# Optimization experiments

Measured on AMD Instinct MI355X. Metric: run time of the kernel, lower is better.

The kernel has to match this reference:

```python
import jax, jax.numpy as jnp
import numpy as np

N, DIM1, DIM2 = 4096, 512, 128

def setup_inputs() -> dict:
    key = jax.random.key(0)
    kx, kw = jax.random.split(key)
    X = jax.random.normal(kx, (N, DIM1), dtype=jnp.float32)
    # original module initializes weight to ones; use randn-scaled for a
    # non-degenerate correctness baseline is NOT faithful -> keep ones.
    weight = jnp.ones((DIM2, DIM1, DIM1), dtype=jnp.float32)
    return {"X": X, "weight": weight}

def reference(X, weight):
    # Y[n,k] = x_n^T W_k x_n  == diagonal of X @ W_k @ X^T, computed directly
    # without materializing the NxN matrix.
    XW = jnp.einsum('ni,kij->nkj', X, weight)   # [N, dim2, dim1]
    Y = jnp.einsum('nkj,nj->nk', XW, X)         # [N, dim2]
    return Y
```

## Files before the change

### kernel.cpp

```cpp
#include <hip/hip_runtime.h>

#define D1 512
#define K2 128

typedef __bf16 bf16_t;
typedef bf16_t bf16x8 __attribute__((ext_vector_type(8)));
typedef bf16_t bf16x4 __attribute__((ext_vector_type(4)));
typedef float  f32x4  __attribute__((ext_vector_type(4)));
typedef float  f32x16 __attribute__((ext_vector_type(16)));

#define WBF_OFF 0ull
#define XBF_OFF 67108864ull
#define WS_NEED 71303168ull

__global__ __launch_bounds__(256)
void prep_w(const float* __restrict__ W, bf16_t* __restrict__ Wbf)
{
    const int k  = blockIdx.x >> 4;
    const int is = blockIdx.x & 15;
    const int t  = threadIdx.x;
    __shared__ float lt[16384];
    char* ltb = (char*)lt;
    {
        const int r  = t >> 3;
        const int cb = (t & 7) * 64;
        const float* src = W + ((size_t)k * D1 + is * 32 + r) * D1 + cb;
        const int sw = (r & 15) << 4;
        #pragma unroll
        for (int c = 0; c < 16; ++c) {
            float4 v = *reinterpret_cast<const float4*>(src + c * 4);
            *reinterpret_cast<float4*>(ltb + r * 2048 + (((cb + c * 4) * 4) ^ sw)) = v;
        }
    }
    __syncthreads();
    bf16_t* out = Wbf + ((size_t)k * 16 + is) * 16384;
    #pragma unroll
    for (int p = 0; p < 8; ++p) {
        const int cc = p * 256 + t;
        const int s  = cc >> 6;
        const int l2 = cc & 63;
        const int il = l2 & 31;
        const int jb = s * 16 + (l2 >> 5) * 8;
        const int sw = (il & 15) << 4;
        bf16x8 h;
        #pragma unroll
        for (int e = 0; e < 8; ++e) {
            float v = *reinterpret_cast<const float*>(ltb + il * 2048 + (((jb + e) * 4) ^ sw));
            h[e] = (bf16_t)v;
        }
        *reinterpret_cast<bf16x8*>(out + (size_t)cc * 8) = h;
    }
}

__global__ __launch_bounds__(256)
void prep_x(const float* __restrict__ X, bf16_t* __restrict__ Xbf)
{
    const int nb2 = blockIdx.x >> 2;
    const int jc  = blockIdx.x & 3;
    const int t   = threadIdx.x;
    __shared__ float xt[16384];
    {
        const int nl = t >> 1;
        const int cb = (t & 1) * 64;
        const float* src = X + ((size_t)nb2 * 128 + nl) * D1 + jc * 128 + cb;
        #pragma unroll
        for (int c = 0; c < 16; ++c) {
            float4 v = *reinterpret_cast<const float4*>(src + c * 4);
            *reinterpret_cast<float4*>(&xt[nl * 128 + cb + c * 4]) = v;
        }
    }
    __syncthreads();
    bf16_t* outx = Xbf + ((size_t)nb2 * 4 + jc) * 16384;
    #pragma unroll
    for (int p = 0; p < 8; ++p) {
        const int cc   = p * 256 + t;
        const int n    = cc >> 4;
        const int slot = cc & 15;
        const int j8   = slot ^ (n & 15);
        bf16x8 h;
        #pragma unroll
        for (int e = 0; e < 8; ++e) h[e] = (bf16_t)xt[n * 128 + j8 * 8 + e];
        *reinterpret_cast<bf16x8*>(outx + (size_t)cc * 8) = h;
    }
}

__global__ __launch_bounds__(512, 2)
void tr_main(const bf16_t* __restrict__ Wbf, const bf16_t* __restrict__ Xbf,
             float* __restrict__ Y)
{
    extern __shared__ char smem[];
    float* red = (float*)(smem + 131072);

    const int bid = blockIdx.x;
    const int k   = ((bid >> 8) << 3) + (bid & 7);
    const int nb2 = (bid >> 3) & 31;

    const int tid = threadIdx.x;
    const int w   = tid >> 6;
    const int l   = tid & 63;
    const int l31 = l & 31;
    const int lh  = l >> 5;

    {
        const bf16_t* src = Xbf + (size_t)nb2 * 65536;
        bf16x8 tmp[16];
        #pragma unroll
        for (int jc = 0; jc < 4; ++jc)
            #pragma unroll
            for (int p = 0; p < 4; ++p) {
                const int ci = (p * 8 + w) * 64 + l;
                tmp[jc * 4 + p] = *reinterpret_cast<const bf16x8*>(
                    src + (size_t)jc * 16384 + (size_t)ci * 8);
            }
        #pragma unroll
        for (int jc = 0; jc < 4; ++jc)
            #pragma unroll
            for (int p = 0; p < 4; ++p) {
                const int ci = (p * 8 + w) * 64 + l;
                *reinterpret_cast<bf16x8*>(smem + jc * 32768 + ci * 16) = tmp[jc * 4 + p];
            }
    }
    __syncthreads();

    const bf16_t* A0 = Wbf + ((size_t)k * 16 + w * 2) * 16384 + (size_t)l * 8;
    const int sw = (l & 15) << 4;

    f32x16 acc[2][4] = {};

    bf16x8 Aq[2][2];
    #pragma unroll
    for (int d = 0; d < 2; ++d) {
        Aq[d][0] = *reinterpret_cast<const bf16x8*>(A0 + (size_t)d * 512);
        Aq[d][1] = *reinterpret_cast<const bf16x8*>(A0 + 16384 + (size_t)d * 512);
    }

    auto bread = [&](bf16x8* dst, int s) {
        const int slot = s >> 3;
        const int ct   = ((s & 7) * 32 + lh * 16) ^ sw;
        #pragma unroll
        for (int fn = 0; fn < 4; ++fn)
            dst[fn] = *reinterpret_cast<const bf16x8*>(
                smem + slot * 32768 + (fn * 32 + l31) * 256 + ct);
    };

    bf16x8 B[2][4];
    bread(B[0], 0);

    #pragma unroll
    for (int s = 0; s < 32; ++s) {
        const int qi = s & 1;
        bf16x8 a0 = Aq[qi][0];
        bf16x8 a1 = Aq[qi][1];
        if (s + 2 < 32) {
            Aq[qi][0] = *reinterpret_cast<const bf16x8*>(A0 + (size_t)(s + 2) * 512);
            Aq[qi][1] = *reinterpret_cast<const bf16x8*>(A0 + 16384 + (size_t)(s + 2) * 512);
        }
        if (s < 31) bread(B[(s + 1) & 1], s + 1);
        __builtin_amdgcn_s_setprio(1);
        #pragma unroll
        for (int fn = 0; fn < 4; ++fn) {
            acc[0][fn] = __builtin_amdgcn_mfma_f32_32x32x16_bf16(a0, B[qi][fn], acc[0][fn], 0, 0, 0);
            acc[1][fn] = __builtin_amdgcn_mfma_f32_32x32x16_bf16(a1, B[qi][fn], acc[1][fn], 0, 0, 0);
        }
        __builtin_amdgcn_s_setprio(0);
    }

    float yp[4] = {0.f, 0.f, 0.f, 0.f};
    #pragma unroll
    for (int mi = 0; mi < 2; ++mi) {
        const int strip = w * 2 + mi;
        const char* base = smem + ((strip >> 2) & 3) * 32768;
        #pragma unroll
        for (int rq = 0; rq < 4; ++rq) {
            const int slot = (strip * 4 + rq) & 15;
            #pragma unroll
            for (int fn = 0; fn < 4; ++fn) {
                const int n = fn * 32 + l31;
                bf16x4 xv = *reinterpret_cast<const bf16x4*>(
                    base + n * 256 + ((slot ^ (n & 15)) << 4) + lh * 8);
                #pragma unroll
                for (int q = 0; q < 4; ++q)
                    yp[fn] += acc[mi][fn][rq * 4 + q] * (float)xv[q];
            }
        }
    }
    #pragma unroll
    for (int fn = 0; fn < 4; ++fn) {
        float v = yp[fn];
        v += __shfl_down(v, 32);
        if (lh == 0) red[w * 128 + fn * 32 + l31] = v;
    }
    __syncthreads();
    if (tid < 128) {
        float s2 = 0.f;
        #pragma unroll
        for (int w2 = 0; w2 < 8; ++w2) s2 += red[w2 * 128 + tid];
        Y[((size_t)nb2 * 128 + tid) * K2 + k] = s2;
    }
}

__global__ __launch_bounds__(512, 2)
void tensor_reduction_kernel(const float* __restrict__ X,
                             const float* __restrict__ W,
                             float* __restrict__ Y)
{
    const int bid = blockIdx.x;
    const int xcd = bid & 7;
    const int rr_ = bid >> 3;
    const int kk  = xcd + 8 * (rr_ >> 4);
    const int nb  = (rr_ & 15) * 256;

    const int tid = threadIdx.x;
    const int wv  = tid >> 6;
    const int ln  = tid & 63;
    const int lg  = ln >> 4;
    const int lr  = ln & 15;

    __shared__ __align__(16) bf16_t Xs[256 * 64];
    __shared__ __align__(16) bf16_t Ws[2][64 * 64];

    bf16x8 afrag[2][16];
    {
        const int srow = tid >> 4;
        const int sj4  = (tid & 15) * 4;
        #pragma unroll
        for (int c = 0; c < 8; ++c) {
            #pragma unroll
            for (int p = 0; p < 8; ++p) {
                const int row = p * 32 + srow;
                float4 v = *reinterpret_cast<const float4*>(
                    X + (size_t)(nb + row) * D1 + c * 64 + sj4);
                bf16x4 h = { (bf16_t)v.x, (bf16_t)v.y, (bf16_t)v.z, (bf16_t)v.w };
                const int byte = row * 128 + ((sj4 * 2) ^ ((row & 7) << 4));
                *reinterpret_cast<bf16x4*>((char*)Xs + byte) = h;
            }
            __syncthreads();
            #pragma unroll
            for (int m = 0; m < 2; ++m) {
                #pragma unroll
                for (int ks = 0; ks < 2; ++ks) {
                    const int row  = wv * 32 + m * 16 + lr;
                    const int byte = row * 128 + ((ks * 64 + lg * 16) ^ ((row & 7) << 4));
                    afrag[m][2 * c + ks] =
                        *reinterpret_cast<const bf16x8*>((const char*)Xs + byte);
                }
            }
            __syncthreads();
        }
    }

    const float* Wk  = W + (size_t)kk * D1 * D1;
    const int irow = tid >> 3;
    const int j8   = (tid & 7) * 8;

    float ypart[2][4] = {{0.f,0.f,0.f,0.f},{0.f,0.f,0.f,0.f}};

    {
        const float* src = Wk + (size_t)irow * D1 + j8;
        float4 u0 = *reinterpret_cast<const float4*>(src);
        float4 u1 = *reinterpret_cast<const float4*>(src + 4);
        bf16x8 h = { (bf16_t)u0.x,(bf16_t)u0.y,(bf16_t)u0.z,(bf16_t)u0.w,
                     (bf16_t)u1.x,(bf16_t)u1.y,(bf16_t)u1.z,(bf16_t)u1.w };
        const int byte = irow * 128 + ((j8 * 2) ^ ((irow & 7) << 4));
        *reinterpret_cast<bf16x8*>((char*)Ws[0] + byte) = h;
    }
    __syncthreads();

    for (int it = 0; it < 8; ++it) {
        f32x4 acc[2][4] = {};
        #pragma unroll
        for (int jcc = 0; jcc < 8; ++jcc) {
            const int tI  = it * 8 + jcc;
            const int cur = tI & 1;
            float4 u0, u1;
            const bool pf = (tI < 63);
            if (pf) {
                const int nit = (tI + 1) >> 3, njc = (tI + 1) & 7;
                const float* src = Wk + (size_t)(nit * 64 + irow) * D1 + njc * 64 + j8;
                u0 = *reinterpret_cast<const float4*>(src);
                u1 = *reinterpret_cast<const float4*>(src + 4);
            }
            #pragma unroll
            for (int ks = 0; ks < 2; ++ks) {
                bf16x8 bfr[4];
                #pragma unroll
                for (int f = 0; f < 4; ++f) {
                    const int ir   = f * 16 + lr;
                    const int byte = ir * 128 + ((ks * 64 + lg * 16) ^ ((ir & 7) << 4));
                    bfr[f] = *reinterpret_cast<const bf16x8*>((const char*)Ws[cur] + byte);
                }
                #pragma unroll
                for (int m = 0; m < 2; ++m)
                    #pragma unroll
                    for (int f = 0; f < 4; ++f)
                        acc[m][f] = __builtin_amdgcn_mfma_f32_16x16x32_bf16(
                            afrag[m][2 * jcc + ks], bfr[f], acc[m][f], 0, 0, 0);
            }
            if (pf) {
                bf16x8 h = { (bf16_t)u0.x,(bf16_t)u0.y,(bf16_t)u0.z,(bf16_t)u0.w,
                             (bf16_t)u1.x,(bf16_t)u1.y,(bf16_t)u1.z,(bf16_t)u1.w };
                const int byte = irow * 128 + ((j8 * 2) ^ ((irow & 7) << 4));
                *reinterpret_cast<bf16x8*>((char*)Ws[cur ^ 1] + byte) = h;
            }
            __syncthreads();
        }
        #pragma unroll
        for (int m = 0; m < 2; ++m) {
            #pragma unroll
            for (int f = 0; f < 4; ++f) {
                const int col = it * 64 + f * 16 + lr;
                #pragma unroll
                for (int q = 0; q < 4; ++q) {
                    const int grow = nb + wv * 32 + m * 16 + lg * 4 + q;
                    ypart[m][q] += acc[m][f][q] * X[(size_t)grow * D1 + col];
                }
            }
        }
    }

    #pragma unroll
    for (int m = 0; m < 2; ++m) {
        #pragma unroll
        for (int q = 0; q < 4; ++q) {
            float v = ypart[m][q];
            v += __shfl_xor(v, 1, 64);
            v += __shfl_xor(v, 2, 64);
            v += __shfl_xor(v, 4, 64);
            v += __shfl_xor(v, 8, 64);
            if (lr == 0) {
                const int grow = nb + wv * 32 + m * 16 + lg * 4 + q;
                Y[(size_t)grow * K2 + kk] = v;
            }
        }
    }
}

extern "C" void kernel_launch(void* const* d_in, const int* in_sizes, int n_in,
                              void* d_out, int out_size, void* d_ws, size_t ws_size,
                              hipStream_t stream)
{
    const float* X = (const float*)d_in[0];
    const float* W = (const float*)d_in[1];
    float* Y = (float*)d_out;

    if (d_ws != nullptr && ws_size >= WS_NEED) {
        bf16_t* Wbf = (bf16_t*)((char*)d_ws + WBF_OFF);
        bf16_t* Xbf = (bf16_t*)((char*)d_ws + XBF_OFF);
        prep_w<<<2048, 256, 0, stream>>>(W, Wbf);
        prep_x<<<128, 256, 0, stream>>>(X, Xbf);
        (void)hipFuncSetAttribute((const void*)tr_main,
                                  hipFuncAttributeMaxDynamicSharedMemorySize, 135168);
        tr_main<<<4096, 512, 135168, stream>>>(Wbf, Xbf, Y);
    } else {
        tensor_reduction_kernel<<<2048, 512, 0, stream>>>(X, W, Y);
    }
}
```

Baseline: 282.6 us.

## Halve tr_main N tile to 64 rows to raise occupancy

Shrinks each tr_main block from 128 to 64 X rows, halving LDS usage and accumulators, doubling the grid to 8192 blocks and raising launch bounds to 4 blocks per CU. The aim is to fit more blocks per CU and hide load latency better. In exchange each bf16 weight tile is reused across half as many rows, so total weight traffic from cache/HBM doubles.

```diff
diff --git a/kernel.cpp b/kernel.cpp
--- a/kernel.cpp
+++ b/kernel.cpp
@@ -84,16 +84,16 @@
     }
 }
 
-__global__ __launch_bounds__(512, 2)
+__global__ __launch_bounds__(512, 4)
 void tr_main(const bf16_t* __restrict__ Wbf, const bf16_t* __restrict__ Xbf,
              float* __restrict__ Y)
 {
     extern __shared__ char smem[];
-    float* red = (float*)(smem + 131072);
+    float* red = (float*)(smem + 65536);
 
     const int bid = blockIdx.x;
-    const int k   = ((bid >> 8) << 3) + (bid & 7);
-    const int nb2 = (bid >> 3) & 31;
+    const int k   = (bid & 7) + ((bid >> 9) << 3);
+    const int nb  = (bid >> 3) & 63;
 
     const int tid = threadIdx.x;
     const int w   = tid >> 6;
@@ -102,22 +102,22 @@
     const int lh  = l >> 5;
 
     {
-        const bf16_t* src = Xbf + (size_t)nb2 * 65536;
-        bf16x8 tmp[16];
+        const bf16_t* src = Xbf + (size_t)(nb >> 1) * 65536 + (size_t)(nb & 1) * 8192;
+        bf16x8 tmp[8];
         #pragma unroll
         for (int jc = 0; jc < 4; ++jc)
             #pragma unroll
-            for (int p = 0; p < 4; ++p) {
-                const int ci = (p * 8 + w) * 64 + l;
-                tmp[jc * 4 + p] = *reinterpret_cast<const bf16x8*>(
+            for (int p = 0; p < 2; ++p) {
+                const int ci = p * 512 + tid;
+                tmp[jc * 2 + p] = *reinterpret_cast<const bf16x8*>(
                     src + (size_t)jc * 16384 + (size_t)ci * 8);
             }
         #pragma unroll
         for (int jc = 0; jc < 4; ++jc)
             #pragma unroll
-            for (int p = 0; p < 4; ++p) {
-                const int ci = (p * 8 + w) * 64 + l;
-                *reinterpret_cast<bf16x8*>(smem + jc * 32768 + ci * 16) = tmp[jc * 4 + p];
+            for (int p = 0; p < 2; ++p) {
+                const int ci = p * 512 + tid;
+                *reinterpret_cast<bf16x8*>(smem + jc * 16384 + ci * 16) = tmp[jc * 2 + p];
             }
     }
     __syncthreads();
@@ -125,7 +125,7 @@
     const bf16_t* A0 = Wbf + ((size_t)k * 16 + w * 2) * 16384 + (size_t)l * 8;
     const int sw = (l & 15) << 4;
 
-    f32x16 acc[2][4] = {};
+    f32x16 acc[2][2] = {};
 
     bf16x8 Aq[2][2];
     #pragma unroll
@@ -134,16 +134,16 @@
         Aq[d][1] = *reinterpret_cast<const bf16x8*>(A0 + 16384 + (size_t)d * 512);
     }
 
-    auto bread = [&](bf16x8* dst, int s) {
-        const int slot = s >> 3;
-        const int ct   = ((s & 7) * 32 + lh * 16) ^ sw;
-        #pragma unroll
-        for (int fn = 0; fn < 4; ++fn)
+    auto bread = [&](bf16x8* dst, int su) {
+        const char* base = smem + (su >> 3) * 16384;
+        const int ct = ((((su & 7) * 2 + lh) << 4)) ^ sw;
+        #pragma unroll
+        for (int fn = 0; fn < 2; ++fn)
             dst[fn] = *reinterpret_cast<const bf16x8*>(
-                smem + slot * 32768 + (fn * 32 + l31) * 256 + ct);
+                base + (fn * 32 + l31) * 256 + ct);
     };
 
-    bf16x8 B[2][4];
+    bf16x8 B[2][2];
     bread(B[0], 0);
 
     #pragma unroll
@@ -157,24 +157,23 @@
         }
         if (s < 31) bread(B[(s + 1) & 1], s + 1);
         __builtin_amdgcn_s_setprio(1);
-        #pragma unroll
-        for (int fn = 0; fn < 4; ++fn) {
-            acc[0][fn] = __builtin_amdgcn_mfma_f32_32x32x16_bf16(a0, B[qi][fn], acc[0][fn], 0, 0, 0);
-            acc[1][fn] = __builtin_amdgcn_mfma_f32_32x32x16_bf16(a1, B[qi][fn], acc[1][fn], 0, 0, 0);
-        }
+        acc[0][0] = __builtin_amdgcn_mfma_f32_32x32x16_bf16(a0, B[qi][0], acc[0][0], 0, 0, 0);
+        acc[0][1] = __builtin_amdgcn_mfma_f32_32x32x16_bf16(a0, B[qi][1], acc[0][1], 0, 0, 0);
+        acc[1][0] = __builtin_amdgcn_mfma_f32_32x32x16_bf16(a1, B[qi][0], acc[1][0], 0, 0, 0);
+        acc[1][1] = __builtin_amdgcn_mfma_f32_32x32x16_bf16(a1, B[qi][1], acc[1][1], 0, 0, 0);
         __builtin_amdgcn_s_setprio(0);
     }
 
-    float yp[4] = {0.f, 0.f, 0.f, 0.f};
+    float yp[2] = {0.f, 0.f};
     #pragma unroll
     for (int mi = 0; mi < 2; ++mi) {
-        const int strip = w * 2 + mi;
-        const char* base = smem + ((strip >> 2) & 3) * 32768;
+        const int st32 = w * 2 + mi;
+        const char* base = smem + (st32 >> 2) * 16384;
         #pragma unroll
         for (int rq = 0; rq < 4; ++rq) {
-            const int slot = (strip * 4 + rq) & 15;
-            #pragma unroll
-            for (int fn = 0; fn < 4; ++fn) {
+            const int slot = (st32 * 4 + rq) & 15;
+            #pragma unroll
+            for (int fn = 0; fn < 2; ++fn) {
                 const int n = fn * 32 + l31;
                 bf16x4 xv = *reinterpret_cast<const bf16x4*>(
                     base + n * 256 + ((slot ^ (n & 15)) << 4) + lh * 8);
@@ -185,17 +184,17 @@
         }
     }
     #pragma unroll
-    for (int fn = 0; fn < 4; ++fn) {
+    for (int fn = 0; fn < 2; ++fn) {
         float v = yp[fn];
         v += __shfl_down(v, 32);
-        if (lh == 0) red[w * 128 + fn * 32 + l31] = v;
-    }
-    __syncthreads();
-    if (tid < 128) {
+        if (lh == 0) red[w * 64 + fn * 32 + l31] = v;
+    }
+    __syncthreads();
+    if (tid < 64) {
         float s2 = 0.f;
         #pragma unroll
-        for (int w2 = 0; w2 < 8; ++w2) s2 += red[w2 * 128 + tid];
-        Y[((size_t)nb2 * 128 + tid) * K2 + k] = s2;
+        for (int w2 = 0; w2 < 8; ++w2) s2 += red[w2 * 64 + tid];
+        Y[((size_t)nb * 64 + tid) * K2 + k] = s2;
     }
 }
 
@@ -349,8 +348,8 @@
         prep_w<<<2048, 256, 0, stream>>>(W, Wbf);
         prep_x<<<128, 256, 0, stream>>>(X, Xbf);
         (void)hipFuncSetAttribute((const void*)tr_main,
-                                  hipFuncAttributeMaxDynamicSharedMemorySize, 135168);
-        tr_main<<<4096, 512, 135168, stream>>>(Wbf, Xbf, Y);
+                                  hipFuncAttributeMaxDynamicSharedMemorySize, 67584);
+        tr_main<<<8192, 512, 67584, stream>>>(Wbf, Xbf, Y);
     } else {
         tensor_reduction_kernel<<<2048, 512, 0, stream>>>(X, W, Y);
     }
```

Result: no change. 278.8 us (-1.3%).

## Double-buffer X tiles via direct global-to-LDS loads, halving shared memory

Applied to the files above, without the earlier changes.

The main kernel stops staging the whole 128KB X tile in LDS up front. It streams 32KB X chunks into two LDS buffers using global_load_lds and overlaps those loads with MFMA work on the other buffer. Each wave now handles one 32-row strip at a time, two sequential passes with an accumulator reset and fold in between, so register use drops and launch bounds allow 4 blocks per CU instead of 2. This trades extra barriers, per-step W loads with no register prefetch, and repeated B reads from LDS for higher occupancy and less upfront load latency.

```diff
diff --git a/kernel.cpp b/kernel.cpp
--- a/kernel.cpp
+++ b/kernel.cpp
@@ -12,6 +12,10 @@
 #define WBF_OFF 0ull
 #define XBF_OFF 67108864ull
 #define WS_NEED 71303168ull
+
+#define GLOAD_LDS16(g, l)  __builtin_amdgcn_global_load_lds(              \
+    (__attribute__((address_space(1))) void*)(g),                         \
+    (__attribute__((address_space(3))) void*)(l), 16, 0, 0)
 
 __global__ __launch_bounds__(256)
 void prep_w(const float* __restrict__ W, bf16_t* __restrict__ Wbf)
@@ -84,106 +88,107 @@
     }
 }
 
-__global__ __launch_bounds__(512, 2)
+__global__ __launch_bounds__(512, 4)
 void tr_main(const bf16_t* __restrict__ Wbf, const bf16_t* __restrict__ Xbf,
              float* __restrict__ Y)
 {
     extern __shared__ char smem[];
-    float* red = (float*)(smem + 131072);
+    float* red = (float*)(smem + 65536);
 
     const int bid = blockIdx.x;
-    const int k   = ((bid >> 8) << 3) + (bid & 7);
-    const int nb2 = (bid >> 3) & 31;
+    const int k   = (bid & 7) + 8 * (bid >> 8);
+    const int nt  = (bid >> 3) & 31;
 
     const int tid = threadIdx.x;
     const int w   = tid >> 6;
     const int l   = tid & 63;
     const int l31 = l & 31;
     const int lh  = l >> 5;
-
-    {
-        const bf16_t* src = Xbf + (size_t)nb2 * 65536;
-        bf16x8 tmp[16];
-        #pragma unroll
-        for (int jc = 0; jc < 4; ++jc)
-            #pragma unroll
-            for (int p = 0; p < 4; ++p) {
-                const int ci = (p * 8 + w) * 64 + l;
-                tmp[jc * 4 + p] = *reinterpret_cast<const bf16x8*>(
-                    src + (size_t)jc * 16384 + (size_t)ci * 8);
-            }
-        #pragma unroll
-        for (int jc = 0; jc < 4; ++jc)
-            #pragma unroll
-            for (int p = 0; p < 4; ++p) {
-                const int ci = (p * 8 + w) * 64 + l;
-                *reinterpret_cast<bf16x8*>(smem + jc * 32768 + ci * 16) = tmp[jc * 4 + p];
-            }
-    }
-    __syncthreads();
-
-    const bf16_t* A0 = Wbf + ((size_t)k * 16 + w * 2) * 16384 + (size_t)l * 8;
-    const int sw = (l & 15) << 4;
-
-    f32x16 acc[2][4] = {};
-
-    bf16x8 Aq[2][2];
-    #pragma unroll
-    for (int d = 0; d < 2; ++d) {
-        Aq[d][0] = *reinterpret_cast<const bf16x8*>(A0 + (size_t)d * 512);
-        Aq[d][1] = *reinterpret_cast<const bf16x8*>(A0 + 16384 + (size_t)d * 512);
-    }
-
-    auto bread = [&](bf16x8* dst, int s) {
-        const int slot = s >> 3;
-        const int ct   = ((s & 7) * 32 + lh * 16) ^ sw;
-        #pragma unroll
-        for (int fn = 0; fn < 4; ++fn)
-            dst[fn] = *reinterpret_cast<const bf16x8*>(
-                smem + slot * 32768 + (fn * 32 + l31) * 256 + ct);
+    const int sw  = (l & 15) << 4;
+
+    const bf16_t* xsrc = Xbf + (size_t)nt * 65536;
+
+    f32x16 acc[4];
+    float  yp[4] = {0.f, 0.f, 0.f, 0.f};
+
+    auto stage = [&](int jc, int buf) {
+        const bf16_t* src = xsrc + (size_t)jc * 16384;
+        char* ldsb = smem + buf * 32768;
+        #pragma unroll
+        for (int q = 0; q < 4; ++q) {
+            const int cb = (q * 8 + w) * 64;
+            GLOAD_LDS16(src + (size_t)(cb + l) * 8, ldsb + (size_t)cb * 16);
+        }
     };
 
-    bf16x8 B[2][4];
-    bread(B[0], 0);
-
-    #pragma unroll
-    for (int s = 0; s < 32; ++s) {
-        const int qi = s & 1;
-        bf16x8 a0 = Aq[qi][0];
-        bf16x8 a1 = Aq[qi][1];
-        if (s + 2 < 32) {
-            Aq[qi][0] = *reinterpret_cast<const bf16x8*>(A0 + (size_t)(s + 2) * 512);
-            Aq[qi][1] = *reinterpret_cast<const bf16x8*>(A0 + 16384 + (size_t)(s + 2) * 512);
-        }
-        if (s < 31) bread(B[(s + 1) & 1], s + 1);
-        __builtin_amdgcn_s_setprio(1);
-        #pragma unroll
-        for (int fn = 0; fn < 4; ++fn) {
-            acc[0][fn] = __builtin_amdgcn_mfma_f32_32x32x16_bf16(a0, B[qi][fn], acc[0][fn], 0, 0, 0);
-            acc[1][fn] = __builtin_amdgcn_mfma_f32_32x32x16_bf16(a1, B[qi][fn], acc[1][fn], 0, 0, 0);
-        }
-        __builtin_amdgcn_s_setprio(0);
-    }
-
-    float yp[4] = {0.f, 0.f, 0.f, 0.f};
-    #pragma unroll
-    for (int mi = 0; mi < 2; ++mi) {
-        const int strip = w * 2 + mi;
-        const char* base = smem + ((strip >> 2) & 3) * 32768;
+    const bf16_t* Abase0 = Wbf + ((size_t)k * 16 + w) * 16384 + (size_t)l * 8;
+
+    auto tile8 = [&](const bf16_t* Ap, int jc, int buf) {
+        const bf16_t* Ab = Ap + (size_t)jc * 4096;
+        const char* base = smem + buf * 32768;
+        #pragma unroll
+        for (int su = 0; su < 8; ++su) {
+            bf16x8 a = *reinterpret_cast<const bf16x8*>(Ab + (size_t)su * 512);
+            const int ct = ((su * 2 + lh) << 4) ^ sw;
+            bf16x8 Bf[4];
+            #pragma unroll
+            for (int fn = 0; fn < 4; ++fn)
+                Bf[fn] = *reinterpret_cast<const bf16x8*>(
+                    base + (fn * 32 + l31) * 256 + ct);
+            #pragma unroll
+            for (int fn = 0; fn < 4; ++fn)
+                acc[fn] = __builtin_amdgcn_mfma_f32_32x32x16_bf16(a, Bf[fn], acc[fn], 0, 0, 0);
+        }
+    };
+
+    auto fold = [&](int p) {
         #pragma unroll
         for (int rq = 0; rq < 4; ++rq) {
-            const int slot = (strip * 4 + rq) & 15;
+            const int db = (p * 8 + w) * 4 + rq;
+            const char* fb = smem + ((db >> 4) & 1) * 32768;
+            const int bl = db & 15;
             #pragma unroll
             for (int fn = 0; fn < 4; ++fn) {
                 const int n = fn * 32 + l31;
                 bf16x4 xv = *reinterpret_cast<const bf16x4*>(
-                    base + n * 256 + ((slot ^ (n & 15)) << 4) + lh * 8);
+                    fb + n * 256 + ((bl ^ (n & 15)) << 4) + lh * 8);
                 #pragma unroll
                 for (int q = 0; q < 4; ++q)
-                    yp[fn] += acc[mi][fn][rq * 4 + q] * (float)xv[q];
-            }
-        }
-    }
+                    yp[fn] += acc[fn][rq * 4 + q] * (float)xv[q];
+            }
+        }
+    };
+
+    auto zacc = [&]() {
+        #pragma unroll
+        for (int fn = 0; fn < 4; ++fn)
+            #pragma unroll
+            for (int e = 0; e < 16; ++e) acc[fn][e] = 0.f;
+    };
+
+    zacc();
+    stage(2, 0);
+    __syncthreads();
+    stage(3, 1); tile8(Abase0, 2, 0);
+    __syncthreads();
+    stage(0, 0); tile8(Abase0, 3, 1);
+    __syncthreads();
+    stage(1, 1); tile8(Abase0, 0, 0);
+    __syncthreads();
+    tile8(Abase0, 1, 1);
+    fold(0);
+
+    const bf16_t* Abase1 = Abase0 + (size_t)8 * 16384;
+    zacc();
+    tile8(Abase1, 0, 0);
+    __syncthreads();
+    stage(2, 0); tile8(Abase1, 1, 1);
+    __syncthreads();
+    stage(3, 1); tile8(Abase1, 2, 0);
+    __syncthreads();
+    tile8(Abase1, 3, 1);
+    fold(1);
+
     #pragma unroll
     for (int fn = 0; fn < 4; ++fn) {
         float v = yp[fn];
@@ -195,7 +200,7 @@
         float s2 = 0.f;
         #pragma unroll
         for (int w2 = 0; w2 < 8; ++w2) s2 += red[w2 * 128 + tid];
-        Y[((size_t)nb2 * 128 + tid) * K2 + k] = s2;
+        Y[((size_t)nt * 128 + tid) * K2 + k] = s2;
     }
 }
 
@@ -349,8 +354,8 @@
         prep_w<<<2048, 256, 0, stream>>>(W, Wbf);
         prep_x<<<128, 256, 0, stream>>>(X, Xbf);
         (void)hipFuncSetAttribute((const void*)tr_main,
-                                  hipFuncAttributeMaxDynamicSharedMemorySize, 135168);
-        tr_main<<<4096, 512, 135168, stream>>>(Wbf, Xbf, Y);
+                                  hipFuncAttributeMaxDynamicSharedMemorySize, 69632);
+        tr_main<<<4096, 512, 69632, stream>>>(Wbf, Xbf, Y);
     } else {
         tensor_reduction_kernel<<<2048, 512, 0, stream>>>(X, W, Y);
     }
```

Measured after the change: 423.7 us. 49.9% more time.
